# Kernel tuning notes

Measured on AMD Instinct MI355X. Metric: run time of the kernel, lower is better.

The kernel has to match this reference:

```python
import jax, jax.numpy as jnp
import numpy as np

B, S, DM, H, D = 4, 2048, 1024, 16, 64
CAP = 15.0
EPS = 1e-6


def setup_inputs() -> dict:
    key = jax.random.key(0)
    ks = jax.random.split(key, 5)
    return {
        "x": jax.random.normal(ks[0], (B, S, DM), jnp.float32),
        "hidden_state": jnp.zeros((B, H, D, D), jnp.float32),
        "w_qkv": jax.random.normal(ks[1], (3 * H * D, DM), jnp.float32) * 0.02,
        "w_gate": jax.random.normal(ks[2], (3 * H, DM), jnp.float32) * 0.02,
        "w_out": jax.random.normal(ks[3], (DM, H * D), jnp.float32) * 0.02,
        "ln_w": jnp.ones((DM,), jnp.float32),
    }


def reference(x, hidden_state, w_qkv, w_gate, w_out, ln_w):
    Bq, Sq, DMq = x.shape
    residual = x
    # RMSNorm (computed in float32, matching the torch module)
    xf = x.astype(jnp.float32)
    var = jnp.mean(xf * xf, axis=-1, keepdims=True)
    xn = ln_w * (xf * jax.lax.rsqrt(var + EPS)).astype(x.dtype)
    # Fused qkv projection: (B,S,3,H,D)
    qkv = jnp.einsum('bsd,od->bso', xn, w_qkv).reshape(Bq, Sq, 3, H, D)
    q, k, v = qkv[:, :, 0], qkv[:, :, 1], qkv[:, :, 2]
    # Gates: (B,S,3,H) -> soft cap -> sigmoid
    gates = jnp.einsum('bsd,od->bso', xn, w_gate).reshape(Bq, Sq, 3, H)
    gates = jax.nn.sigmoid(CAP * jnp.tanh(gates / CAP))
    ig, fg, og = gates[:, :, 0], gates[:, :, 1], gates[:, :, 2]

    def step(h, inp):
        q_t, k_t, v_t, i_t, f_t, o_t = inp  # q/k/v: (B,H,D); gates: (B,H)
        kv = jnp.einsum('bhd,bhe->bhde', k_t, v_t)
        h = f_t[..., None, None] * h + i_t[..., None, None] * kv
        out = o_t[..., None] * jnp.einsum('bhd,bhde->bhe', q_t, h)
        return h, out

    xs = (q.swapaxes(0, 1), k.swapaxes(0, 1), v.swapaxes(0, 1),
          ig.swapaxes(0, 1), fg.swapaxes(0, 1), og.swapaxes(0, 1))
    h_final, outs = jax.lax.scan(step, hidden_state, xs)  # outs: (S,B,H,D)
    output = outs.swapaxes(0, 1).reshape(Bq, Sq, H * D)
    y = residual + output @ w_out.T
    return y, h_final
```

## Files before the change

### kernel.cpp

```cpp
#include <hip/hip_runtime.h>
#include <hip/hip_bf16.h>
#include <math.h>
#include <stdint.h>

#define Bq 4
#define Sq 2048
#define DMq 1024
#define Hq 16
#define Dq 64
#define CAPf 15.0f
#define EPSf 1e-6f
#define Tc 64
#define Cc (Sq / Tc)
#define QKVW (3 * Hq * Dq)
#define NGATE (3 * Hq)
#define NMERGE (QKVW + NGATE)
#define NPAD 3328

typedef __attribute__((ext_vector_type(8))) short short8;
typedef __attribute__((ext_vector_type(4))) float f32x4;
typedef __hip_bfloat16 bf16;

__device__ __forceinline__ float b2f(bf16 v) { return __bfloat162float(v); }
__device__ __forceinline__ bf16  f2b(float v) { return __float2bfloat16(v); }
__device__ __forceinline__ uint16_t f2bu(float f) {
    bf16 h = __float2bfloat16(f); uint16_t u; __builtin_memcpy(&u, &h, 2); return u;
}
__device__ __forceinline__ float bu2f(uint16_t u) {
    uint32_t x = ((uint32_t)u) << 16; float f; __builtin_memcpy(&f, &x, 4); return f;
}

__global__ void convert_all(const float* __restrict__ wqkv,
                            const float* __restrict__ wgate,
                            const float* __restrict__ wout,
                            bf16* __restrict__ wcomb, bf16* __restrict__ wob) {
    const int n1 = QKVW * DMq / 4;
    const int n2 = (NPAD - QKVW) * DMq / 4;
    const int ng = NGATE * DMq / 4;
    const int n3 = DMq * Hq * Dq / 4;
    int i = blockIdx.x * 256 + threadIdx.x;
    if (i < n1) {
        float4 v = ((const float4*)wqkv)[i];
        bf16 t[4] = {f2b(v.x), f2b(v.y), f2b(v.z), f2b(v.w)};
        ((uint2*)wcomb)[i] = *(uint2*)t;
    } else if (i < n1 + n2) {
        int j = i - n1;
        uint2 o = make_uint2(0u, 0u);
        if (j < ng) {
            float4 v = ((const float4*)wgate)[j];
            bf16 t[4] = {f2b(v.x), f2b(v.y), f2b(v.z), f2b(v.w)};
            o = *(uint2*)t;
        }
        ((uint2*)wcomb)[n1 + j] = o;
    } else if (i < n1 + n2 + n3) {
        int j = i - n1 - n2;
        float4 v = ((const float4*)wout)[j];
        bf16 t[4] = {f2b(v.x), f2b(v.y), f2b(v.z), f2b(v.w)};
        ((uint2*)wob)[j] = *(uint2*)t;
    }
}

__global__ void rmsnorm_kernel(const float* __restrict__ x,
                               const float* __restrict__ ln_w,
                               bf16* __restrict__ xn) {
    int row = blockIdx.x;
    const float4* xr = (const float4*)(x + (size_t)row * DMq);
    int tid = threadIdx.x;
    float4 v = xr[tid];
    float ss = v.x*v.x + v.y*v.y + v.z*v.z + v.w*v.w;
    #pragma unroll
    for (int off = 32; off > 0; off >>= 1) ss += __shfl_down(ss, off);
    __shared__ float red[4];
    int lane = tid & 63, wv = tid >> 6;
    if (lane == 0) red[wv] = ss;
    __syncthreads();
    float tot = red[0] + red[1] + red[2] + red[3];
    float rs = rsqrtf(tot * (1.0f / DMq) + EPSf);
    float4 w4 = ((const float4*)ln_w)[tid];
    bf16 t[4] = {f2b(v.x * rs * w4.x), f2b(v.y * rs * w4.y),
                 f2b(v.z * rs * w4.z), f2b(v.w * rs * w4.w)};
    *(uint2*)(xn + (size_t)row * DMq + tid * 4) = *(uint2*)t;
}

__global__ __launch_bounds__(512, 2) void gemm_qkvgate(const bf16* __restrict__ A,
                                                       const bf16* __restrict__ Bw,
                                                       bf16* __restrict__ qkvb,
                                                       float* __restrict__ gates) {
    __shared__ bf16 lds[2][2][256 * 64];
    const int tid = threadIdx.x;
    const int w = tid >> 6;
    const int l = tid & 63;
    const int wrow = (w >> 2) * 128;
    const int wcol = (w & 3) * 64;
    const int bm = blockIdx.y * 256;
    const int bn = blockIdx.x * 256;

    const int lrow = l >> 3;
    const int swzc = ((l & 7) ^ lrow) * 8;
    const int fl = l & 15;
    const int kb = l >> 4;
    const int rsw = l & 7;

    f32x4 acc[8][4];
    #pragma unroll
    for (int i = 0; i < 8; i++)
        #pragma unroll
        for (int j = 0; j < 4; j++) acc[i][j] = (f32x4){0.f, 0.f, 0.f, 0.f};

    auto stage = [&](int slot, int kt) {
        const int k0 = kt * 64;
        #pragma unroll
        for (int inst = 0; inst < 4; inst++) {
            int r0 = w * 32 + inst * 8;
            const bf16* gp = A + (size_t)(bm + r0 + lrow) * DMq + k0 + swzc;
            __builtin_amdgcn_global_load_lds(
                (const __attribute__((address_space(1))) uint32_t*)gp,
                (__attribute__((address_space(3))) uint32_t*)(&lds[slot][0][r0 * 64]),
                16, 0, 0);
        }
        #pragma unroll
        for (int inst = 0; inst < 4; inst++) {
            int r0 = w * 32 + inst * 8;
            const bf16* gp = Bw + (size_t)(bn + r0 + lrow) * DMq + k0 + swzc;
            __builtin_amdgcn_global_load_lds(
                (const __attribute__((address_space(1))) uint32_t*)gp,
                (__attribute__((address_space(3))) uint32_t*)(&lds[slot][1][r0 * 64]),
                16, 0, 0);
        }
    };

    auto compute_half = [&](int slot) {
        const bf16* As_ = &lds[slot][0][0];
        const bf16* Bs_ = &lds[slot][1][0];
        short8 bfrag[4][2];
        #pragma unroll
        for (int j = 0; j < 4; j++)
            #pragma unroll
            for (int kk = 0; kk < 2; kk++) {
                int row = wcol + j * 16 + fl;
                bfrag[j][kk] = *(const short8*)(Bs_ + row * 64 + (((kk << 2) + kb) ^ rsw) * 8);
            }
        #pragma unroll
        for (int q = 0; q < 4; q++) {
            short8 af[2][2];
            #pragma unroll
            for (int ii = 0; ii < 2; ii++)
                #pragma unroll
                for (int kk = 0; kk < 2; kk++) {
                    int row = wrow + (q * 2 + ii) * 16 + fl;
                    af[ii][kk] = *(const short8*)(As_ + row * 64 + (((kk << 2) + kb) ^ rsw) * 8);
                }
            __builtin_amdgcn_s_setprio(1);
            #pragma unroll
            for (int ii = 0; ii < 2; ii++)
                #pragma unroll
                for (int j = 0; j < 4; j++)
                    #pragma unroll
                    for (int kk = 0; kk < 2; kk++)
                        acc[q * 2 + ii][j] = __builtin_amdgcn_mfma_f32_16x16x32_bf16(
                            af[ii][kk], bfrag[j][kk], acc[q * 2 + ii][j], 0, 0, 0);
            __builtin_amdgcn_s_setprio(0);
        }
    };

    stage(0, 0);
    asm volatile("s_waitcnt vmcnt(0)" ::: "memory");
    __builtin_amdgcn_s_barrier();
    __builtin_amdgcn_sched_barrier(0);

    #pragma unroll 1
    for (int it = 0; it < 8; it++) {
        stage(1, 2 * it + 1);
        compute_half(0);
        asm volatile("s_waitcnt vmcnt(0)" ::: "memory");
        __builtin_amdgcn_s_barrier();
        __builtin_amdgcn_sched_barrier(0);
        if (it < 7) stage(0, 2 * it + 2);
        compute_half(1);
        asm volatile("s_waitcnt vmcnt(0)" ::: "memory");
        __builtin_amdgcn_s_barrier();
        __builtin_amdgcn_sched_barrier(0);
    }

    #pragma unroll
    for (int i = 0; i < 8; i++) {
        #pragma unroll
        for (int j = 0; j < 4; j++) {
            int col = bn + wcol + j * 16 + fl;
            #pragma unroll
            for (int r = 0; r < 4; r++) {
                int row = bm + wrow + i * 16 + kb * 4 + r;
                float v = acc[i][j][r];
                if (col < QKVW) {
                    qkvb[(size_t)row * QKVW + col] = f2b(v);
                } else if (col < NMERGE) {
                    float g = CAPf * tanhf(v * (1.0f / CAPf));
                    gates[(size_t)row * NGATE + (col - QKVW)] = 1.0f / (1.0f + expf(-g));
                }
            }
        }
    }
}

__global__ __launch_bounds__(256) void gemm_out(const bf16* __restrict__ A,
                                                const bf16* __restrict__ Bw,
                                                const float* __restrict__ resid,
                                                float* __restrict__ C,
                                                int M, int N, int K) {
    __shared__ bf16 As[128 * 64];
    __shared__ bf16 Bs[128 * 64];
    const int tid = threadIdx.x;
    const int w = tid >> 6;
    const int l = tid & 63;
    const int wr = (w >> 1) * 64;
    const int wc = (w & 1) * 64;
    const int bm = blockIdx.y * 128;
    const int bn = blockIdx.x * 128;

    const int lrow = l >> 3;
    const int swzc = ((l & 7) ^ lrow) * 8;
    const int fl = l & 15;
    const int kb = l >> 4;
    const int rsw = l & 7;

    f32x4 acc[4][4];
    #pragma unroll
    for (int i = 0; i < 4; i++)
        #pragma unroll
        for (int j = 0; j < 4; j++) acc[i][j] = (f32x4){0.f, 0.f, 0.f, 0.f};

    for (int k0 = 0; k0 < K; k0 += 64) {
        __syncthreads();
        #pragma unroll
        for (int inst = 0; inst < 4; inst++) {
            int r0 = w * 32 + inst * 8;
            const bf16* gp = A + (size_t)(bm + r0 + lrow) * K + k0 + swzc;
            __builtin_amdgcn_global_load_lds(
                (const __attribute__((address_space(1))) uint32_t*)gp,
                (__attribute__((address_space(3))) uint32_t*)(As + r0 * 64),
                16, 0, 0);
        }
        #pragma unroll
        for (int inst = 0; inst < 4; inst++) {
            int r0 = w * 32 + inst * 8;
            const bf16* gp = Bw + (size_t)(bn + r0 + lrow) * K + k0 + swzc;
            __builtin_amdgcn_global_load_lds(
                (const __attribute__((address_space(1))) uint32_t*)gp,
                (__attribute__((address_space(3))) uint32_t*)(Bs + r0 * 64),
                16, 0, 0);
        }
        __syncthreads();
        #pragma unroll
        for (int kk2 = 0; kk2 < 2; kk2++) {
            const int koff = (((kk2 << 2) + kb) ^ rsw) * 8;
            short8 af[4], bfr[4];
            #pragma unroll
            for (int i = 0; i < 4; i++)
                af[i] = *(const short8*)(As + (wr + i * 16 + fl) * 64 + koff);
            #pragma unroll
            for (int j = 0; j < 4; j++)
                bfr[j] = *(const short8*)(Bs + (wc + j * 16 + fl) * 64 + koff);
            #pragma unroll
            for (int i = 0; i < 4; i++)
                #pragma unroll
                for (int j = 0; j < 4; j++)
                    acc[i][j] = __builtin_amdgcn_mfma_f32_16x16x32_bf16(
                        af[i], bfr[j], acc[i][j], 0, 0, 0);
        }
    }

    #pragma unroll
    for (int i = 0; i < 4; i++) {
        #pragma unroll
        for (int j = 0; j < 4; j++) {
            int col = bn + wc + j * 16 + fl;
            #pragma unroll
            for (int r = 0; r < 4; r++) {
                int row = bm + wr + i * 16 + kb * 4 + r;
                size_t idx = (size_t)row * N + col;
                C[idx] = acc[i][j][r] + resid[idx];
            }
        }
    }
}

__global__ __launch_bounds__(64) void chunk_intra(const bf16* __restrict__ qkvb,
                                                  const float* __restrict__ gates,
                                                  bf16* __restrict__ attb,
                                                  bf16* __restrict__ LT,
                                                  float* __restrict__ oaArr,
                                                  float* __restrict__ Fch) {
    const int blk = blockIdx.x;
    const int c  = blk & (Cc - 1);
    const int bh = blk >> 5;
    const int b = bh >> 4, hh = bh & 15;
    const int l = threadIdx.x;
    const int s0 = c * Tc;

    __shared__ bf16 KTs[4096];
    __shared__ bf16 VTs[4096];
    __shared__ bf16 Ps[4096];
    __shared__ float rowS[64], pcolS[64], wstS[64];

    const float* gp = gates + (size_t)(b * Sq + s0 + l) * NGATE;
    float ig = gp[hh], fg = gp[Hq + hh], og = gp[2 * Hq + hh];
    float la = __logf(fg);
    #pragma unroll
    for (int off = 1; off < 64; off <<= 1) {
        float v = __shfl_up(la, off);
        if (l >= off) la += v;
    }
    float la63 = __shfl(la, 63);
    float li = __logf(ig);
    rowS[l]  = la + __logf(og);
    pcolS[l] = li - la;
    wstS[l]  = __expf(la63 - la + li);
    float oa = og * __expf(la);
    oaArr[(size_t)blk * 64 + l] = oa;
    if (l == 0) Fch[blk] = __expf(la63);
    __syncthreads();

    const int cg = l & 7, rp = l >> 3;
    const size_t rowBase = (size_t)(b * Sq + s0);
    const int kcol = (Hq + hh) * Dq, vcol = (2 * Hq + hh) * Dq;
    #pragma unroll
    for (int pass = 0; pass < 4; pass++) {
        int j0 = pass * 16 + rp * 2;
        const bf16* r0 = qkvb + (rowBase + j0) * QKVW;
        const bf16* r1 = qkvb + (rowBase + j0 + 1) * QKVW;
        short8 k0 = *(const short8*)(r0 + kcol + cg * 8);
        short8 k1 = *(const short8*)(r1 + kcol + cg * 8);
        short8 v0 = *(const short8*)(r0 + vcol + cg * 8);
        short8 v1 = *(const short8*)(r1 + vcol + cg * 8);
        float w0 = wstS[j0], w1 = wstS[j0 + 1];
        #pragma unroll
        for (int s = 0; s < 8; s++) {
            int cc = cg * 8 + s;
            int base = cc * 64 + ((((j0 >> 3) ^ (cc & 7) ^ (cc >> 3))) << 3) + (j0 & 7);
            uint32_t kp = (uint32_t)f2bu(bu2f((uint16_t)k0[s]) * w0)
                        | ((uint32_t)f2bu(bu2f((uint16_t)k1[s]) * w1) << 16);
            uint32_t vp = (uint32_t)(uint16_t)v0[s] | ((uint32_t)(uint16_t)v1[s] << 16);
            *(uint32_t*)&KTs[base] = kp;
            *(uint32_t*)&VTs[base] = vp;
        }
    }

    const int fl = l & 15, kb = l >> 4;
    const bf16* Qb = qkvb + rowBase * QKVW + hh * Dq;
    const bf16* Kb = qkvb + rowBase * QKVW + kcol;
    f32x4 accS[4][4];
    #pragma unroll
    for (int i = 0; i < 4; i++)
        #pragma unroll
        for (int j = 0; j < 4; j++) accS[i][j] = (f32x4){0.f, 0.f, 0.f, 0.f};
    #pragma unroll
    for (int ks = 0; ks < 2; ks++) {
        short8 qf[4], kf[4];
        #pragma unroll
        for (int i = 0; i < 4; i++)
            qf[i] = *(const short8*)(Qb + (size_t)(i * 16 + fl) * QKVW + ks * 32 + kb * 8);
        #pragma unroll
        for (int j = 0; j < 4; j++)
            kf[j] = *(const short8*)(Kb + (size_t)(j * 16 + fl) * QKVW + ks * 32 + kb * 8);
        #pragma unroll
        for (int i = 0; i < 4; i++)
            #pragma unroll
            for (int j = 0; j < 4; j++)
                accS[i][j] = __builtin_amdgcn_mfma_f32_16x16x32_bf16(qf[i], kf[j], accS[i][j], 0, 0, 0);
    }

    #pragma unroll
    for (int i = 0; i < 4; i++) {
        #pragma unroll
        for (int j = 0; j < 4; j++) {
            int jj = j * 16 + fl;
            float pc = pcolS[jj];
            #pragma unroll
            for (int r = 0; r < 4; r++) {
                int t = i * 16 + kb * 4 + r;
                float p = (jj <= t) ? __expf(rowS[t] + pc) * accS[i][j][r] : 0.f;
                int slot = (jj >> 3) ^ (t & 7) ^ (t >> 3);
                Ps[t * 64 + slot * 8 + (jj & 7)] = f2b(p);
            }
        }
    }
    __syncthreads();

    f32x4 accO[4][4], accL[4][4];
    #pragma unroll
    for (int i = 0; i < 4; i++)
        #pragma unroll
        for (int j = 0; j < 4; j++) {
            accO[i][j] = (f32x4){0.f, 0.f, 0.f, 0.f};
            accL[i][j] = (f32x4){0.f, 0.f, 0.f, 0.f};
        }
    #pragma unroll
    for (int ks = 0; ks < 2; ks++) {
        short8 pf[4], vt[4], kt[4];
        #pragma unroll
        for (int i = 0; i < 4; i++) {
            int row = i * 16 + fl;
            int koff = (((ks * 4 + kb) ^ (row & 7) ^ (row >> 3))) << 3;
            pf[i] = *(const short8*)(Ps  + row * 64 + koff);
            vt[i] = *(const short8*)(VTs + row * 64 + koff);
            kt[i] = *(const short8*)(KTs + row * 64 + koff);
        }
        #pragma unroll
        for (int i = 0; i < 4; i++)
            #pragma unroll
            for (int j = 0; j < 4; j++) {
                accO[i][j] = __builtin_amdgcn_mfma_f32_16x16x32_bf16(pf[i], vt[j], accO[i][j], 0, 0, 0);
                accL[i][j] = __builtin_amdgcn_mfma_f32_16x16x32_bf16(vt[i], kt[j], accL[i][j], 0, 0, 0);
            }
    }

    #pragma unroll
    for (int i = 0; i < 4; i++)
        #pragma unroll
        for (int j = 0; j < 4; j++)
            #pragma unroll
            for (int r = 0; r < 4; r++) {
                int rr = i * 16 + kb * 4 + r, cc2 = j * 16 + fl;
                attb[(rowBase + rr) * (Hq * Dq) + hh * Dq + cc2] = f2b(accO[i][j][r]);
                LT[(size_t)blk * 4096 + rr * 64 + cc2] = f2b(accL[i][j][r]);
            }
}

__global__ __launch_bounds__(256) void scan_pass2(bf16* __restrict__ LH,
                                                  const float* __restrict__ Fchunk,
                                                  const float* __restrict__ h0,
                                                  float* __restrict__ hfin) {
    int idx = blockIdx.x * 256 + threadIdx.x;
    int bh = idx >> 12;
    int ed = idx & 4095;
    int e = ed >> 6, d = ed & 63;
    float run = h0[(size_t)bh * 4096 + d * 64 + e];
    #pragma unroll
    for (int c = 0; c < Cc; c++) {
        float Fv = Fchunk[bh * Cc + c];
        size_t off = ((size_t)bh * Cc + c) * 4096 + ed;
        float Lv = b2f(LH[off]);
        LH[off] = f2b(run);
        run = Fv * run + Lv;
    }
    hfin[(size_t)bh * 4096 + d * 64 + e] = run;
}

__global__ __launch_bounds__(64) void chunk_cross(const bf16* __restrict__ qkvb,
                                                  const bf16* __restrict__ HT,
                                                  const float* __restrict__ oaArr,
                                                  bf16* __restrict__ attb) {
    const int blk = blockIdx.x;
    const int c = blk & (Cc - 1);
    const int bh = blk >> 5;
    const int b = bh >> 4, hh = bh & 15;
    const int l = threadIdx.x, fl = l & 15, kb = l >> 4;
    const size_t rowBase = (size_t)(b * Sq + c * Tc);
    __shared__ float oaS[64];
    oaS[l] = oaArr[(size_t)blk * 64 + l];
    __syncthreads();
    const bf16* Qb = qkvb + rowBase * QKVW + hh * Dq;
    const bf16* Hb = HT + (size_t)blk * 4096;
    f32x4 acc[4][4];
    #pragma unroll
    for (int i = 0; i < 4; i++)
        #pragma unroll
        for (int j = 0; j < 4; j++) acc[i][j] = (f32x4){0.f, 0.f, 0.f, 0.f};
    #pragma unroll
    for (int ks = 0; ks < 2; ks++) {
        short8 qf[4], hf[4];
        #pragma unroll
        for (int i = 0; i < 4; i++)
            qf[i] = *(const short8*)(Qb + (size_t)(i * 16 + fl) * QKVW + ks * 32 + kb * 8);
        #pragma unroll
        for (int j = 0; j < 4; j++)
            hf[j] = *(const short8*)(Hb + (j * 16 + fl) * 64 + ks * 32 + kb * 8);
        #pragma unroll
        for (int i = 0; i < 4; i++)
            #pragma unroll
            for (int j = 0; j < 4; j++)
                acc[i][j] = __builtin_amdgcn_mfma_f32_16x16x32_bf16(qf[i], hf[j], acc[i][j], 0, 0, 0);
    }
    #pragma unroll
    for (int i = 0; i < 4; i++)
        #pragma unroll
        for (int j = 0; j < 4; j++)
            #pragma unroll
            for (int r = 0; r < 4; r++) {
                int t = i * 16 + kb * 4 + r, e = j * 16 + fl;
                size_t idx = (rowBase + t) * (Hq * Dq) + hh * Dq + e;
                attb[idx] = f2b(b2f(attb[idx]) + oaS[t] * acc[i][j][r]);
            }
}

extern "C" void kernel_launch(void* const* d_in, const int* in_sizes, int n_in,
                              void* d_out, int out_size, void* d_ws, size_t ws_size,
                              hipStream_t stream) {
    const float* x      = (const float*)d_in[0];
    const float* h0     = (const float*)d_in[1];
    const float* w_qkv  = (const float*)d_in[2];
    const float* w_gate = (const float*)d_in[3];
    const float* w_out  = (const float*)d_in[4];
    const float* ln_w   = (const float*)d_in[5];

    const size_t MS = (size_t)Bq * Sq;
    const size_t BH = (size_t)Bq * Hq;

    float* p = (float*)d_ws;
    bf16*  xnb   = (bf16*)p;  p += MS * DMq / 2;
    bf16*  qkvb  = (bf16*)p;  p += MS * QKVW / 2;
    float* gates = p;         p += MS * NGATE;
    float* oaArr = p;         p += BH * Cc * Tc;
    float* Fch   = p;         p += BH * Cc;
    bf16*  LT    = (bf16*)p;  p += BH * Cc * Dq * Dq / 2;
    bf16*  wcomb = (bf16*)p;  p += (size_t)NPAD * DMq / 2;
    bf16*  wob   = (bf16*)p;  p += (size_t)DMq * Hq * Dq / 2;
    size_t need = (size_t)(p - (float*)d_ws) * sizeof(float);
    if (ws_size < need) return;
    bf16* attb = xnb;

    float* y    = (float*)d_out;
    float* hfin = y + MS * DMq;

    const int cvt_n = (QKVW * DMq + (NPAD - QKVW) * DMq + DMq * Hq * Dq) / 4;
    convert_all<<<dim3((cvt_n + 255) / 256), dim3(256), 0, stream>>>(
        w_qkv, w_gate, w_out, wcomb, wob);

    rmsnorm_kernel<<<dim3(MS), dim3(256), 0, stream>>>(x, ln_w, xnb);

    gemm_qkvgate<<<dim3(NPAD / 256, MS / 256), dim3(512), 0, stream>>>(
        xnb, wcomb, qkvb, gates);

    chunk_intra<<<dim3(BH * Cc), dim3(64), 0, stream>>>(qkvb, gates, attb, LT, oaArr, Fch);
    scan_pass2<<<dim3(BH * 4096 / 256), dim3(256), 0, stream>>>(LT, Fch, h0, hfin);
    chunk_cross<<<dim3(BH * Cc), dim3(64), 0, stream>>>(qkvb, LT, oaArr, attb);

    gemm_out<<<dim3(DMq / 128, MS / 128), dim3(256), 0, stream>>>(
        attb, wob, x, y, (int)MS, DMq, Hq * Dq);
}
```

Baseline: 187.3 us.

## Shrink QKV-gate GEMM to single-buffered 128x128 tiles with tighter N padding

Replaces the 256x256, 512-thread, double-buffered QKV/gate GEMM with a simpler 128x128, 256-thread, single-buffered version that synchronizes before and after each K tile. The padded output width drops from 3328 to 3200, since 3200 is a multiple of 128 that still covers the 3120 merged columns, which cuts wasted columns. The smaller tiles give more blocks for better CU coverage on the 8192x3200 problem. In exchange, the kernel loses the overlap between global loads and MFMA compute and gets less data reuse per tile.

```diff
diff --git a/kernel.cpp b/kernel.cpp
--- a/kernel.cpp
+++ b/kernel.cpp
@@ -15,7 +15,7 @@
 #define QKVW (3 * Hq * Dq)
 #define NGATE (3 * Hq)
 #define NMERGE (QKVW + NGATE)
-#define NPAD 3328
+#define NPAD 3200
 
 typedef __attribute__((ext_vector_type(8))) short short8;
 typedef __attribute__((ext_vector_type(4))) float f32x4;
@@ -82,18 +82,19 @@
     *(uint2*)(xn + (size_t)row * DMq + tid * 4) = *(uint2*)t;
 }
 
-__global__ __launch_bounds__(512, 2) void gemm_qkvgate(const bf16* __restrict__ A,
-                                                       const bf16* __restrict__ Bw,
-                                                       bf16* __restrict__ qkvb,
-                                                       float* __restrict__ gates) {
-    __shared__ bf16 lds[2][2][256 * 64];
+__global__ __launch_bounds__(256) void gemm_qkvgate(const bf16* __restrict__ A,
+                                                    const bf16* __restrict__ Bw,
+                                                    bf16* __restrict__ qkvb,
+                                                    float* __restrict__ gates) {
+    __shared__ bf16 As[128 * 64];
+    __shared__ bf16 Bs[128 * 64];
     const int tid = threadIdx.x;
     const int w = tid >> 6;
     const int l = tid & 63;
-    const int wrow = (w >> 2) * 128;
-    const int wcol = (w & 3) * 64;
-    const int bm = blockIdx.y * 256;
-    const int bn = blockIdx.x * 256;
+    const int wr = (w >> 1) * 64;
+    const int wc = (w & 1) * 64;
+    const int bm = blockIdx.y * 128;
+    const int bn = blockIdx.x * 128;
 
     const int lrow = l >> 3;
     const int swzc = ((l & 7) ^ lrow) * 8;
@@ -101,21 +102,21 @@
     const int kb = l >> 4;
     const int rsw = l & 7;
 
-    f32x4 acc[8][4];
-    #pragma unroll
-    for (int i = 0; i < 8; i++)
+    f32x4 acc[4][4];
+    #pragma unroll
+    for (int i = 0; i < 4; i++)
         #pragma unroll
         for (int j = 0; j < 4; j++) acc[i][j] = (f32x4){0.f, 0.f, 0.f, 0.f};
 
-    auto stage = [&](int slot, int kt) {
-        const int k0 = kt * 64;
+    for (int k0 = 0; k0 < DMq; k0 += 64) {
+        __syncthreads();
         #pragma unroll
         for (int inst = 0; inst < 4; inst++) {
             int r0 = w * 32 + inst * 8;
             const bf16* gp = A + (size_t)(bm + r0 + lrow) * DMq + k0 + swzc;
             __builtin_amdgcn_global_load_lds(
                 (const __attribute__((address_space(1))) uint32_t*)gp,
-                (__attribute__((address_space(3))) uint32_t*)(&lds[slot][0][r0 * 64]),
+                (__attribute__((address_space(3))) uint32_t*)(As + r0 * 64),
                 16, 0, 0);
         }
         #pragma unroll
@@ -124,72 +125,37 @@
             const bf16* gp = Bw + (size_t)(bn + r0 + lrow) * DMq + k0 + swzc;
             __builtin_amdgcn_global_load_lds(
                 (const __attribute__((address_space(1))) uint32_t*)gp,
-                (__attribute__((address_space(3))) uint32_t*)(&lds[slot][1][r0 * 64]),
+                (__attribute__((address_space(3))) uint32_t*)(Bs + r0 * 64),
                 16, 0, 0);
         }
-    };
-
-    auto compute_half = [&](int slot) {
-        const bf16* As_ = &lds[slot][0][0];
-        const bf16* Bs_ = &lds[slot][1][0];
-        short8 bfrag[4][2];
-        #pragma unroll
-        for (int j = 0; j < 4; j++)
-            #pragma unroll
-            for (int kk = 0; kk < 2; kk++) {
-                int row = wcol + j * 16 + fl;
-                bfrag[j][kk] = *(const short8*)(Bs_ + row * 64 + (((kk << 2) + kb) ^ rsw) * 8);
-            }
-        #pragma unroll
-        for (int q = 0; q < 4; q++) {
-            short8 af[2][2];
-            #pragma unroll
-            for (int ii = 0; ii < 2; ii++)
-                #pragma unroll
-                for (int kk = 0; kk < 2; kk++) {
-                    int row = wrow + (q * 2 + ii) * 16 + fl;
-                    af[ii][kk] = *(const short8*)(As_ + row * 64 + (((kk << 2) + kb) ^ rsw) * 8);
-                }
-            __builtin_amdgcn_s_setprio(1);
-            #pragma unroll
-            for (int ii = 0; ii < 2; ii++)
+        __syncthreads();
+        #pragma unroll
+        for (int kk2 = 0; kk2 < 2; kk2++) {
+            const int koff = (((kk2 << 2) + kb) ^ rsw) * 8;
+            short8 af[4], bfr[4];
+            #pragma unroll
+            for (int i = 0; i < 4; i++)
+                af[i] = *(const short8*)(As + (wr + i * 16 + fl) * 64 + koff);
+            #pragma unroll
+            for (int j = 0; j < 4; j++)
+                bfr[j] = *(const short8*)(Bs + (wc + j * 16 + fl) * 64 + koff);
+            #pragma unroll
+            for (int i = 0; i < 4; i++)
                 #pragma unroll
                 for (int j = 0; j < 4; j++)
-                    #pragma unroll
-                    for (int kk = 0; kk < 2; kk++)
-                        acc[q * 2 + ii][j] = __builtin_amdgcn_mfma_f32_16x16x32_bf16(
-                            af[ii][kk], bfrag[j][kk], acc[q * 2 + ii][j], 0, 0, 0);
-            __builtin_amdgcn_s_setprio(0);
-        }
-    };
-
-    stage(0, 0);
-    asm volatile("s_waitcnt vmcnt(0)" ::: "memory");
-    __builtin_amdgcn_s_barrier();
-    __builtin_amdgcn_sched_barrier(0);
-
-    #pragma unroll 1
-    for (int it = 0; it < 8; it++) {
-        stage(1, 2 * it + 1);
-        compute_half(0);
-        asm volatile("s_waitcnt vmcnt(0)" ::: "memory");
-        __builtin_amdgcn_s_barrier();
-        __builtin_amdgcn_sched_barrier(0);
-        if (it < 7) stage(0, 2 * it + 2);
-        compute_half(1);
-        asm volatile("s_waitcnt vmcnt(0)" ::: "memory");
-        __builtin_amdgcn_s_barrier();
-        __builtin_amdgcn_sched_barrier(0);
-    }
-
-    #pragma unroll
-    for (int i = 0; i < 8; i++) {
+                    acc[i][j] = __builtin_amdgcn_mfma_f32_16x16x32_bf16(
+                        af[i], bfr[j], acc[i][j], 0, 0, 0);
+        }
+    }
+
+    #pragma unroll
+    for (int i = 0; i < 4; i++) {
         #pragma unroll
         for (int j = 0; j < 4; j++) {
-            int col = bn + wcol + j * 16 + fl;
+            int col = bn + wc + j * 16 + fl;
             #pragma unroll
             for (int r = 0; r < 4; r++) {
-                int row = bm + wrow + i * 16 + kb * 4 + r;
+                int row = bm + wr + i * 16 + kb * 4 + r;
                 float v = acc[i][j][r];
                 if (col < QKVW) {
                     qkvb[(size_t)row * QKVW + col] = f2b(v);
@@ -528,7 +494,7 @@
 
     rmsnorm_kernel<<<dim3(MS), dim3(256), 0, stream>>>(x, ln_w, xnb);
 
-    gemm_qkvgate<<<dim3(NPAD / 256, MS / 256), dim3(512), 0, stream>>>(
+    gemm_qkvgate<<<dim3(NPAD / 128, MS / 128), dim3(256), 0, stream>>>(
         xnb, wcomb, qkvb, gates);
 
     chunk_intra<<<dim3(BH * Cc), dim3(64), 0, stream>>>(qkvb, gates, attb, LT, oaArr, Fch);
```

New measurement: 192.6 us. 2.8% more time.
